# Performance work log

Hardware: AMD Instinct MI355X
Metric: run time of the kernel (lower is better)

## Reference

```python
import jax, jax.numpy as jnp
import numpy as np

B, T, D, H, HD, L, V = 2048, 64, 128, 4, 32, 6, 256
DFF = 4 * D
PARAM_NAMES = ['tok_emb', 'pos_emb', 'Wq', 'Wk', 'Wv', 'Wo', 'bo', 'ln1_g', 'ln1_b',
               'W1', 'b1', 'W2', 'b2', 'ln2_g', 'ln2_b', 'lnf_g', 'lnf_b', 'Wh', 'bh']


def setup_inputs() -> dict:
    key = jax.random.key(0)
    ks = jax.random.split(key, 12)
    def n(k, shape, s=0.02):
        return jax.random.normal(k, shape, jnp.float32) * s
    return dict(
        idx=jax.random.randint(ks[0], (B, T), 0, V),
        tok_emb=n(ks[1], (V, D)),
        pos_emb=n(ks[2], (T, D)),
        Wq=n(ks[3], (L, H, D, HD)),
        Wk=n(ks[4], (L, H, D, HD)),
        Wv=n(ks[5], (L, H, D, HD)),
        Wo=n(ks[6], (L, D, D)), bo=jnp.zeros((L, D), jnp.float32),
        ln1_g=jnp.ones((L, D), jnp.float32), ln1_b=jnp.zeros((L, D), jnp.float32),
        W1=n(ks[7], (L, D, DFF)), b1=jnp.zeros((L, DFF), jnp.float32),
        W2=n(ks[8], (L, DFF, D)), b2=jnp.zeros((L, D), jnp.float32),
        ln2_g=jnp.ones((L, D), jnp.float32), ln2_b=jnp.zeros((L, D), jnp.float32),
        lnf_g=jnp.ones((D,), jnp.float32), lnf_b=jnp.zeros((D,), jnp.float32),
        Wh=n(ks[9], (D, V)), bh=jnp.zeros((V,), jnp.float32),
    )


def _ln(x, g, b):
    m = x.mean(-1, keepdims=True)
    v = x.var(-1, keepdims=True)  # biased, matches torch LayerNorm
    return (x - m) / jnp.sqrt(v + 1e-5) * g + b


def _forward(idx, p):
    x = p['tok_emb'][idx] + p['pos_emb'][None, :, :]  # [B,T,D]
    mask = jnp.tril(jnp.ones((T, T), bool))

    def block(x, lp):
        Wq, Wk, Wv, Wo, bo, g1, bb1, W1, b1, W2, b2, g2, bb2 = lp
        h = _ln(x, g1, bb1)
        q = jnp.einsum('btd,hde->bhte', h, Wq)
        k = jnp.einsum('btd,hde->bhte', h, Wk)
        v = jnp.einsum('btd,hde->bhte', h, Wv)
        s = jnp.einsum('bhte,bhse->bhts', q, k) * (HD ** -0.5)
        s = jnp.where(mask, s, -jnp.inf)
        w = jax.nn.softmax(s, axis=-1)  # dropout inactive (eval mode)
        o = jnp.einsum('bhts,bhse->bthe', w, v).reshape(B, T, D)  # concat heads
        x = x + o @ Wo + bo
        h2 = _ln(x, g2, bb2)
        x = x + jax.nn.relu(h2 @ W1 + b1) @ W2 + b2
        return x, None

    lp = (p['Wq'], p['Wk'], p['Wv'], p['Wo'], p['bo'], p['ln1_g'], p['ln1_b'],
          p['W1'], p['b1'], p['W2'], p['b2'], p['ln2_g'], p['ln2_b'])
    x, _ = jax.lax.scan(block, x, lp)
    x = _ln(x, p['lnf_g'], p['lnf_b'])
    return x @ p['Wh'] + p['bh']  # [B,T,V] logits


def reference(idx, tok_emb, pos_emb, Wq, Wk, Wv, Wo, bo, ln1_g, ln1_b,
              W1, b1, W2, b2, ln2_g, ln2_b, lnf_g, lnf_b, Wh, bh):
    p = dict(zip(PARAM_NAMES, (tok_emb, pos_emb, Wq, Wk, Wv, Wo, bo, ln1_g, ln1_b,
                               W1, b1, W2, b2, ln2_g, ln2_b, lnf_g, lnf_b, Wh, bh)))
    return _forward(idx, p)
```

## Files before the change

### kernel.cpp

```cpp
#include <hip/hip_runtime.h>

typedef unsigned short ushort_t;
typedef __attribute__((ext_vector_type(8))) short short8;
typedef __attribute__((ext_vector_type(4))) float float4_;

#define B_   2048
#define T_   64
#define D_   128
#define H_   4
#define HD_  32
#define L_   6
#define V_   256
#define DFF_ 512
#define BT_  (B_*T_)

static __device__ __forceinline__ float b2f(ushort_t u) {
    return __uint_as_float(((unsigned int)u) << 16);
}
static __device__ __forceinline__ ushort_t f2b(float f) {
    unsigned int x = __float_as_uint(f);
    return (ushort_t)((x + 0x7fffu + ((x >> 16) & 1u)) >> 16);
}
static __device__ __forceinline__ int bf16_mode(const ushort_t* flag_src) {
    return flag_src[0] == 0x3F80;
}

#define AS1C(p) ((const __attribute__((address_space(1))) void*)(p))
#define AS3(p)  ((__attribute__((address_space(3))) void*)(p))

#define NCVT 19
struct Cvt {
    const void* src[NCVT];
    long base[NCVT];
    long total;
};

__global__ __launch_bounds__(256) void convert_all(
    Cvt c, ushort_t* __restrict__ dst, const ushort_t* __restrict__ flag_src)
{
    long i = (long)blockIdx.x * 256 + threadIdx.x;
    if (i >= c.total) return;
    int s = 0;
    #pragma unroll 1
    while (s + 1 < NCVT && i >= c.base[s + 1]) s++;
    long j = i - c.base[s];
    if (bf16_mode(flag_src))
        dst[i] = ((const ushort_t*)c.src[s])[j];
    else
        dst[i] = f2b(((const float*)c.src[s])[j]);
}

__global__ __launch_bounds__(256) void repack_qkv(
    const ushort_t* __restrict__ Wq, const ushort_t* __restrict__ Wk,
    const ushort_t* __restrict__ Wv, ushort_t* __restrict__ outw)
{
    int i = blockIdx.x * 256 + threadIdx.x;
    int d = i & 127;
    int c = (i >> 7) % 384;
    int l = i / (384 * 128);
    int sel = c >> 7, hh = (c >> 5) & 3, e = c & 31;
    const ushort_t* W = (sel == 0) ? Wq : (sel == 1) ? Wk : Wv;
    outw[i] = W[((l * 4 + hh) * 128 + d) * 32 + e];
}

__global__ __launch_bounds__(256) void transpose_w(
    const ushort_t* __restrict__ in, ushort_t* __restrict__ out, int K, int N)
{
    long i = (long)blockIdx.x * 256 + threadIdx.x;
    int n = (int)(i % N);
    int k = (int)((i / N) % K);
    int l = (int)(i / ((long)N * K));
    out[((long)l * N + n) * K + k] = in[i];
}

__global__ __launch_bounds__(256) void embed_ln_kernel(
    const int* __restrict__ idx, const ushort_t* __restrict__ tok,
    const ushort_t* __restrict__ pos, const ushort_t* __restrict__ g,
    const ushort_t* __restrict__ bta, float* __restrict__ x,
    ushort_t* __restrict__ hout)
{
    int row  = blockIdx.x * 4 + (threadIdx.x >> 6);
    int lane = threadIdx.x & 63;
    int t = row & 63;
    int id = idx[row];
    float v0 = b2f(tok[id * 128 + lane])      + b2f(pos[t * 128 + lane]);
    float v1 = b2f(tok[id * 128 + lane + 64]) + b2f(pos[t * 128 + lane + 64]);
    long o = (long)row * 128 + lane;
    x[o] = v0; x[o + 64] = v1;
    float s  = v0 + v1;
    float sq = v0 * v0 + v1 * v1;
    #pragma unroll
    for (int off = 1; off < 64; off <<= 1) {
        s  += __shfl_xor(s,  off);
        sq += __shfl_xor(sq, off);
    }
    float mean = s * (1.0f / 128.0f);
    float var  = sq * (1.0f / 128.0f) - mean * mean;
    float rstd = rsqrtf(var + 1e-5f);
    hout[o]      = f2b((v0 - mean) * rstd * b2f(g[lane])      + b2f(bta[lane]));
    hout[o + 64] = f2b((v1 - mean) * rstd * b2f(g[lane + 64]) + b2f(bta[lane + 64]));
}

__global__ __launch_bounds__(256) void gemm_bt(
    const ushort_t* __restrict__ A, const ushort_t* __restrict__ Bt,
    const ushort_t* __restrict__ bias, void* __restrict__ outp,
    const ushort_t* __restrict__ flag, int M, int N, int K, int relu)
{
    __shared__ __align__(16) ushort_t As[128 * 64];
    __shared__ __align__(16) ushort_t Bs[128 * 64];
    const int tid  = threadIdx.x;
    const int wave = tid >> 6, lane = tid & 63;
    const int wm = wave >> 1, wn = wave & 1;
    const int row0 = blockIdx.x * 128, col0 = blockIdx.y * 128;

    float4_ acc[4][4];
    #pragma unroll
    for (int m = 0; m < 4; m++)
        #pragma unroll
        for (int n = 0; n < 4; n++) acc[m][n] = (float4_)0.0f;

    const int srow = lane >> 3;
    const int scg  = (lane & 7) ^ srow;
    const int fr = lane & 15, fq = lane >> 4;

    for (int k0 = 0; k0 < K; k0 += 64) {
        __syncthreads();
        #pragma unroll
        for (int i = 0; i < 4; i++) {
            int chunk = wave * 4 + i;
            int r = chunk * 8 + srow;
            __builtin_amdgcn_global_load_lds(
                AS1C(&A[(size_t)(row0 + r) * K + k0 + scg * 8]),
                AS3(&As[chunk * 512]), 16, 0, 0);
            __builtin_amdgcn_global_load_lds(
                AS1C(&Bt[(size_t)(col0 + r) * K + k0 + scg * 8]),
                AS3(&Bs[chunk * 512]), 16, 0, 0);
        }
        __syncthreads();

        #pragma unroll
        for (int ks = 0; ks < 2; ks++) {
            short8 af[4], bf[4];
            #pragma unroll
            for (int mt = 0; mt < 4; mt++) {
                int r = wm * 64 + mt * 16 + fr;
                af[mt] = *(const short8*)&As[r * 64 + (((ks * 4 + fq) ^ (r & 7)) * 8)];
            }
            #pragma unroll
            for (int nt = 0; nt < 4; nt++) {
                int r = wn * 64 + nt * 16 + fr;
                bf[nt] = *(const short8*)&Bs[r * 64 + (((ks * 4 + fq) ^ (r & 7)) * 8)];
            }
            #pragma unroll
            for (int mt = 0; mt < 4; mt++)
                #pragma unroll
                for (int nt = 0; nt < 4; nt++)
                    acc[mt][nt] = __builtin_amdgcn_mfma_f32_16x16x32_bf16(
                        af[mt], bf[nt], acc[mt][nt], 0, 0, 0);
        }
    }

    const int out_bf16 = (flag == nullptr) || bf16_mode(flag);
    #pragma unroll
    for (int nt = 0; nt < 4; nt++) {
        int gcol = col0 + wn * 64 + nt * 16 + fr;
        float bb = bias ? b2f(bias[gcol]) : 0.0f;
        #pragma unroll
        for (int mt = 0; mt < 4; mt++) {
            #pragma unroll
            for (int i = 0; i < 4; i++) {
                int grow = row0 + wm * 64 + mt * 16 + fq * 4 + i;
                float v = acc[mt][nt][i] + bb;
                if (relu) v = fmaxf(v, 0.0f);
                long off = (long)grow * N + gcol;
                if (out_bf16) ((ushort_t*)outp)[off] = f2b(v);
                else          ((float*)outp)[off] = v;
            }
        }
    }
}

__global__ __launch_bounds__(256) void gemm_ln(
    const ushort_t* __restrict__ A, const ushort_t* __restrict__ Bt,
    const ushort_t* __restrict__ bias, float* __restrict__ x,
    const ushort_t* __restrict__ g, const ushort_t* __restrict__ bta,
    ushort_t* __restrict__ hout, int M, int K)
{
    __shared__ __align__(16) ushort_t As[128 * 64];
    __shared__ __align__(16) ushort_t Bs[128 * 64];
    __shared__ float stats[128][2][2];
    const int tid  = threadIdx.x;
    const int wave = tid >> 6, lane = tid & 63;
    const int wm = wave >> 1, wn = wave & 1;
    const int row0 = blockIdx.x * 128;
    const int N = 128;

    float4_ acc[4][4];
    #pragma unroll
    for (int m = 0; m < 4; m++)
        #pragma unroll
        for (int n = 0; n < 4; n++) acc[m][n] = (float4_)0.0f;

    const int srow = lane >> 3;
    const int scg  = (lane & 7) ^ srow;
    const int fr = lane & 15, fq = lane >> 4;

    for (int k0 = 0; k0 < K; k0 += 64) {
        __syncthreads();
        #pragma unroll
        for (int i = 0; i < 4; i++) {
            int chunk = wave * 4 + i;
            int r = chunk * 8 + srow;
            __builtin_amdgcn_global_load_lds(
                AS1C(&A[(size_t)(row0 + r) * K + k0 + scg * 8]),
                AS3(&As[chunk * 512]), 16, 0, 0);
            __builtin_amdgcn_global_load_lds(
                AS1C(&Bt[(size_t)r * K + k0 + scg * 8]),
                AS3(&Bs[chunk * 512]), 16, 0, 0);
        }
        __syncthreads();

        #pragma unroll
        for (int ks = 0; ks < 2; ks++) {
            short8 af[4], bf[4];
            #pragma unroll
            for (int mt = 0; mt < 4; mt++) {
                int r = wm * 64 + mt * 16 + fr;
                af[mt] = *(const short8*)&As[r * 64 + (((ks * 4 + fq) ^ (r & 7)) * 8)];
            }
            #pragma unroll
            for (int nt = 0; nt < 4; nt++) {
                int r = wn * 64 + nt * 16 + fr;
                bf[nt] = *(const short8*)&Bs[r * 64 + (((ks * 4 + fq) ^ (r & 7)) * 8)];
            }
            #pragma unroll
            for (int mt = 0; mt < 4; mt++)
                #pragma unroll
                for (int nt = 0; nt < 4; nt++)
                    acc[mt][nt] = __builtin_amdgcn_mfma_f32_16x16x32_bf16(
                        af[mt], bf[nt], acc[mt][nt], 0, 0, 0);
        }
    }

    int   col[4];
    float bbias[4], gg[4], bln[4];
    #pragma unroll
    for (int nt = 0; nt < 4; nt++) {
        col[nt]  = wn * 64 + nt * 16 + fr;
        bbias[nt] = b2f(bias[col[nt]]);
        gg[nt]    = b2f(g[col[nt]]);
        bln[nt]   = b2f(bta[col[nt]]);
    }
    #pragma unroll
    for (int mt = 0; mt < 4; mt++) {
        #pragma unroll
        for (int i = 0; i < 4; i++) {
            int lr = wm * 64 + mt * 16 + fq * 4 + i;
            long rbase = (long)(row0 + lr) * N;
            float s = 0.0f, sq = 0.0f;
            #pragma unroll
            for (int nt = 0; nt < 4; nt++) {
                float nx = x[rbase + col[nt]] + acc[mt][nt][i] + bbias[nt];
                x[rbase + col[nt]] = nx;
                acc[mt][nt][i] = nx;
                s += nx; sq += nx * nx;
            }
            s  += __shfl_xor(s, 1);  sq += __shfl_xor(sq, 1);
            s  += __shfl_xor(s, 2);  sq += __shfl_xor(sq, 2);
            s  += __shfl_xor(s, 4);  sq += __shfl_xor(sq, 4);
            s  += __shfl_xor(s, 8);  sq += __shfl_xor(sq, 8);
            if (fr == 0) { stats[lr][wn][0] = s; stats[lr][wn][1] = sq; }
        }
    }
    __syncthreads();
    #pragma unroll
    for (int mt = 0; mt < 4; mt++) {
        #pragma unroll
        for (int i = 0; i < 4; i++) {
            int lr = wm * 64 + mt * 16 + fq * 4 + i;
            float s  = stats[lr][0][0] + stats[lr][1][0];
            float sq = stats[lr][0][1] + stats[lr][1][1];
            float mean = s * (1.0f / 128.0f);
            float var  = sq * (1.0f / 128.0f) - mean * mean;
            float rstd = rsqrtf(var + 1e-5f);
            long rbase = (long)(row0 + lr) * N;
            #pragma unroll
            for (int nt = 0; nt < 4; nt++) {
                float nx = acc[mt][nt][i];
                hout[rbase + col[nt]] = f2b((nx - mean) * rstd * gg[nt] + bln[nt]);
            }
        }
    }
}

__global__ __launch_bounds__(256) void ffn_fused(
    const ushort_t* __restrict__ hin,
    const ushort_t* __restrict__ w1,
    const ushort_t* __restrict__ b1v,
    const ushort_t* __restrict__ w2,
    const ushort_t* __restrict__ b2v,
    float* __restrict__ x,
    const ushort_t* __restrict__ g, const ushort_t* __restrict__ bta,
    ushort_t* __restrict__ hout)
{
    __shared__ __align__(16) ushort_t Hs[128 * 128];
    __shared__ __align__(16) ushort_t Ms[128 * 128];
    __shared__ __align__(16) ushort_t Bs[128 * 64];
    const int tid  = threadIdx.x;
    const int wave = tid >> 6, lane = tid & 63;
    const int wm = wave >> 1, wn = wave & 1;
    const int row0 = blockIdx.x * 128;

    const int srow = lane >> 3;
    const int scg  = (lane & 7) ^ srow;
    const int fr = lane & 15, fq = lane >> 4;

    {
        int lr4 = lane >> 4, pg = lane & 15;
        #pragma unroll
        for (int i = 0; i < 8; i++) {
            int c = wave * 8 + i;
            int r = c * 4 + lr4;
            int kg = pg ^ (r & 7);
            __builtin_amdgcn_global_load_lds(
                AS1C(&hin[(size_t)(row0 + r) * 128 + kg * 8]),
                AS3(&Hs[c * 512]), 16, 0, 0);
        }
    }

    float4_ acc2[4][4];
    #pragma unroll
    for (int m = 0; m < 4; m++)
        #pragma unroll
        for (int n = 0; n < 4; n++) acc2[m][n] = (float4_)0.0f;

    #pragma unroll 1
    for (int c = 0; c < 4; c++) {
        const ushort_t* Wc = w1 + (size_t)c * 128 * 128;
        float4_ acc1[4][4];
        #pragma unroll
        for (int m = 0; m < 4; m++)
            #pragma unroll
            for (int n = 0; n < 4; n++) acc1[m][n] = (float4_)0.0f;

        #pragma unroll 1
        for (int k0 = 0; k0 < 128; k0 += 64) {
            __syncthreads();
            #pragma unroll
            for (int i = 0; i < 4; i++) {
                int chunk = wave * 4 + i;
                int r = chunk * 8 + srow;
                __builtin_amdgcn_global_load_lds(
                    AS1C(&Wc[(size_t)r * 128 + k0 + scg * 8]),
                    AS3(&Bs[chunk * 512]), 16, 0, 0);
            }
            __syncthreads();
            #pragma unroll
            for (int ks = 0; ks < 2; ks++) {
                int kb = (k0 >> 5) + ks;
                short8 af[4], bf[4];
                #pragma unroll
                for (int mt = 0; mt < 4; mt++) {
                    int r = wm * 64 + mt * 16 + fr;
                    af[mt] = *(const short8*)&Hs[r * 128 + (((kb * 4 + fq) ^ (r & 7)) * 8)];
                }
                #pragma unroll
                for (int nt = 0; nt < 4; nt++) {
                    int r = wn * 64 + nt * 16 + fr;
                    bf[nt] = *(const short8*)&Bs[r * 64 + (((ks * 4 + fq) ^ (r & 7)) * 8)];
                }
                #pragma unroll
                for (int mt = 0; mt < 4; mt++)
                    #pragma unroll
                    for (int nt = 0; nt < 4; nt++)
                        acc1[mt][nt] = __builtin_amdgcn_mfma_f32_16x16x32_bf16(
                            af[mt], bf[nt], acc1[mt][nt], 0, 0, 0);
            }
        }

        #pragma unroll
        for (int nt = 0; nt < 4; nt++) {
            int col = wn * 64 + nt * 16 + fr;
            float bb = b2f(b1v[c * 128 + col]);
            #pragma unroll
            for (int mt = 0; mt < 4; mt++) {
                #pragma unroll
                for (int i = 0; i < 4; i++) {
                    int row = wm * 64 + mt * 16 + fq * 4 + i;
                    float v = fmaxf(acc1[mt][nt][i] + bb, 0.0f);
                    Ms[row * 128 + (((col >> 3) ^ (row & 7)) * 8) + (col & 7)] = f2b(v);
                }
            }
        }

        #pragma unroll 1
        for (int k0 = 0; k0 < 128; k0 += 64) {
            __syncthreads();
            #pragma unroll
            for (int i = 0; i < 4; i++) {
                int chunk = wave * 4 + i;
                int r = chunk * 8 + srow;
                __builtin_amdgcn_global_load_lds(
                    AS1C(&w2[(size_t)r * 512 + c * 128 + k0 + scg * 8]),
                    AS3(&Bs[chunk * 512]), 16, 0, 0);
            }
            __syncthreads();
            #pragma unroll
            for (int ks = 0; ks < 2; ks++) {
                int kb = (k0 >> 5) + ks;
                short8 af[4], bf[4];
                #pragma unroll
                for (int mt = 0; mt < 4; mt++) {
                    int r = wm * 64 + mt * 16 + fr;
                    af[mt] = *(const short8*)&Ms[r * 128 + (((kb * 4 + fq) ^ (r & 7)) * 8)];
                }
                #pragma unroll
                for (int nt = 0; nt < 4; nt++) {
                    int r = wn * 64 + nt * 16 + fr;
                    bf[nt] = *(const short8*)&Bs[r * 64 + (((ks * 4 + fq) ^ (r & 7)) * 8)];
                }
                #pragma unroll
                for (int mt = 0; mt < 4; mt++)
                    #pragma unroll
                    for (int nt = 0; nt < 4; nt++)
                        acc2[mt][nt] = __builtin_amdgcn_mfma_f32_16x16x32_bf16(
                            af[mt], bf[nt], acc2[mt][nt], 0, 0, 0);
            }
        }
    }

    __syncthreads();
    float (*stats)[2][2] = (float (*)[2][2])(void*)Bs;
    int   col[4];
    float bbias[4], gg[4], bln[4];
    #pragma unroll
    for (int nt = 0; nt < 4; nt++) {
        col[nt]  = wn * 64 + nt * 16 + fr;
        bbias[nt] = b2f(b2v[col[nt]]);
        gg[nt]    = b2f(g[col[nt]]);
        bln[nt]   = b2f(bta[col[nt]]);
    }
    #pragma unroll
    for (int mt = 0; mt < 4; mt++) {
        #pragma unroll
        for (int i = 0; i < 4; i++) {
            int lr = wm * 64 + mt * 16 + fq * 4 + i;
            long rbase = (long)(row0 + lr) * 128;
            float s = 0.0f, sq = 0.0f;
            #pragma unroll
            for (int nt = 0; nt < 4; nt++) {
                float nx = x[rbase + col[nt]] + acc2[mt][nt][i] + bbias[nt];
                x[rbase + col[nt]] = nx;
                acc2[mt][nt][i] = nx;
                s += nx; sq += nx * nx;
            }
            s  += __shfl_xor(s, 1);  sq += __shfl_xor(sq, 1);
            s  += __shfl_xor(s, 2);  sq += __shfl_xor(sq, 2);
            s  += __shfl_xor(s, 4);  sq += __shfl_xor(sq, 4);
            s  += __shfl_xor(s, 8);  sq += __shfl_xor(sq, 8);
            if (fr == 0) { stats[lr][wn][0] = s; stats[lr][wn][1] = sq; }
        }
    }
    __syncthreads();
    #pragma unroll
    for (int mt = 0; mt < 4; mt++) {
        #pragma unroll
        for (int i = 0; i < 4; i++) {
            int lr = wm * 64 + mt * 16 + fq * 4 + i;
            float s  = stats[lr][0][0] + stats[lr][1][0];
            float sq = stats[lr][0][1] + stats[lr][1][1];
            float mean = s * (1.0f / 128.0f);
            float var  = sq * (1.0f / 128.0f) - mean * mean;
            float rstd = rsqrtf(var + 1e-5f);
            long rbase = (long)(row0 + lr) * 128;
            #pragma unroll
            for (int nt = 0; nt < 4; nt++) {
                float nx = acc2[mt][nt][i];
                hout[rbase + col[nt]] = f2b((nx - mean) * rstd * gg[nt] + bln[nt]);
            }
        }
    }
}

__global__ __launch_bounds__(256) void attn_kernel(
    const ushort_t* __restrict__ qkv,
    ushort_t* __restrict__ out)
{
    __shared__ __align__(16) ushort_t Qs[64][40];
    __shared__ __align__(16) ushort_t Ks[64][40];
    __shared__ __align__(16) ushort_t Vt[32][72];
    __shared__ __align__(16) ushort_t Pb[64][72];
    const int tid = threadIdx.x;
    const int b = blockIdx.x >> 2, h = blockIdx.x & 3;
    const long base = (long)b * T_ * 384 + h * 32;

    {
        int t = tid >> 2, e8 = (tid & 3) * 8;
        const ushort_t* p = &qkv[base + (long)t * 384 + e8];
        short8 qv = *(const short8*)(p);
        short8 kv = *(const short8*)(p + 128);
        short8 vv = *(const short8*)(p + 256);
        *(short8*)&Qs[t][e8] = qv;
        *(short8*)&Ks[t][e8] = kv;
        #pragma unroll
        for (int j = 0; j < 8; j++) Vt[e8 + j][t] = (ushort_t)vv[j];
    }
    __syncthreads();

    const int w = tid >> 6, lane = tid & 63, fr = lane & 15, fq = lane >> 4;

    short8 qf = *(const short8*)&Qs[w * 16 + fr][fq * 8];
    float4_ s[4];
    #pragma unroll
    for (int tj = 0; tj < 4; tj++) s[tj] = (float4_)0.0f;
    #pragma unroll
    for (int tj = 0; tj < 4; tj++) {
        if (tj <= w) {
            short8 kf = *(const short8*)&Ks[tj * 16 + fr][fq * 8];
            s[tj] = __builtin_amdgcn_mfma_f32_16x16x32_bf16(qf, kf, s[tj], 0, 0, 0);
        }
    }

    const float scale = 0.17677669529663687f;
    float pv[4][4];
    #pragma unroll
    for (int i = 0; i < 4; i++) {
        float mx = -1.0e30f;
        float vv4[4];
        int   ok[4];
        #pragma unroll
        for (int tj = 0; tj < 4; tj++) {
            ok[tj] = (tj < w) || (tj == w && fr <= fq * 4 + i);
            float v = ok[tj] ? s[tj][i] * scale : -1.0e30f;
            vv4[tj] = v;
            mx = fmaxf(mx, v);
        }
        mx = fmaxf(mx, __shfl_xor(mx, 1));
        mx = fmaxf(mx, __shfl_xor(mx, 2));
        mx = fmaxf(mx, __shfl_xor(mx, 4));
        mx = fmaxf(mx, __shfl_xor(mx, 8));
        float sm = 0.0f;
        #pragma unroll
        for (int tj = 0; tj < 4; tj++) {
            float e = ok[tj] ? __expf(vv4[tj] - mx) : 0.0f;
            vv4[tj] = e;
            sm += e;
        }
        sm += __shfl_xor(sm, 1);
        sm += __shfl_xor(sm, 2);
        sm += __shfl_xor(sm, 4);
        sm += __shfl_xor(sm, 8);
        float inv = 1.0f / sm;
        #pragma unroll
        for (int tj = 0; tj < 4; tj++) pv[i][tj] = vv4[tj] * inv;
    }
    #pragma unroll
    for (int tj = 0; tj < 4; tj++)
        #pragma unroll
        for (int i = 0; i < 4; i++)
            Pb[w * 16 + fq * 4 + i][tj * 16 + fr] = f2b(pv[i][tj]);
    __syncthreads();

    float4_ o[2];
    o[0] = (float4_)0.0f; o[1] = (float4_)0.0f;
    #pragma unroll
    for (int ks = 0; ks < 2; ks++) {
        short8 pf = *(const short8*)&Pb[w * 16 + fr][ks * 32 + fq * 8];
        #pragma unroll
        for (int nt = 0; nt < 2; nt++) {
            short8 vf = *(const short8*)&Vt[nt * 16 + fr][ks * 32 + fq * 8];
            o[nt] = __builtin_amdgcn_mfma_f32_16x16x32_bf16(pf, vf, o[nt], 0, 0, 0);
        }
    }
    #pragma unroll
    for (int nt = 0; nt < 2; nt++)
        #pragma unroll
        for (int i = 0; i < 4; i++)
            out[(long)(b * T_ + w * 16 + fq * 4 + i) * 128 + h * 32 + nt * 16 + fr]
                = f2b(o[nt][i]);
}

extern "C" void kernel_launch(void* const* d_in, const int* in_sizes, int n_in,
                              void* d_out, int out_size, void* d_ws, size_t ws_size,
                              hipStream_t stream)
{
    (void)in_sizes; (void)n_in; (void)out_size; (void)ws_size;
    const int* idx = (const int*)d_in[0];
    const ushort_t* flag = (const ushort_t*)d_in[8];

    char* ws = (char*)d_ws;
    float*    x    = (float*)ws;     ws += (size_t)BT_ * D_ * 4;
    ushort_t* h    = (ushort_t*)ws;  ws += (size_t)BT_ * D_ * 2;
    ushort_t* qkvb = (ushort_t*)ws;  ws += (size_t)BT_ * 384 * 2;
    ushort_t* ao   = (ushort_t*)ws;  ws += (size_t)BT_ * D_ * 2;
    ushort_t* wqkv = (ushort_t*)ws;  ws += (size_t)L_ * 384 * 128 * 2;
    ushort_t* wo   = (ushort_t*)ws;  ws += (size_t)L_ * 128 * 128 * 2;
    ushort_t* w1   = (ushort_t*)ws;  ws += (size_t)L_ * 512 * 128 * 2;
    ushort_t* w2   = (ushort_t*)ws;  ws += (size_t)L_ * 128 * 512 * 2;
    ushort_t* wh   = (ushort_t*)ws;  ws += (size_t)256 * 128 * 2;
    ushort_t* cvt  = (ushort_t*)ws;

    static const long cnt[NCVT] = {
        (long)V_*D_, (long)T_*D_,
        (long)L_*H_*D_*HD_, (long)L_*H_*D_*HD_, (long)L_*H_*D_*HD_,
        (long)L_*D_*D_, (long)L_*D_,
        (long)L_*D_, (long)L_*D_,
        (long)L_*D_*DFF_, (long)L_*DFF_,
        (long)L_*DFF_*D_, (long)L_*D_,
        (long)L_*D_, (long)L_*D_,
        (long)D_, (long)D_,
        (long)D_*V_, (long)V_
    };
    Cvt c;
    long off = 0;
    for (int i = 0; i < NCVT; i++) { c.src[i] = d_in[i + 1]; c.base[i] = off; off += cnt[i]; }
    c.total = off;
    ushort_t* ctok  = cvt + c.base[0];
    ushort_t* cpos  = cvt + c.base[1];
    ushort_t* cWq   = cvt + c.base[2];
    ushort_t* cWk   = cvt + c.base[3];
    ushort_t* cWv   = cvt + c.base[4];
    ushort_t* cWo   = cvt + c.base[5];
    ushort_t* cbo   = cvt + c.base[6];
    ushort_t* cln1g = cvt + c.base[7];
    ushort_t* cln1b = cvt + c.base[8];
    ushort_t* cW1   = cvt + c.base[9];
    ushort_t* cb1   = cvt + c.base[10];
    ushort_t* cW2   = cvt + c.base[11];
    ushort_t* cb2   = cvt + c.base[12];
    ushort_t* cln2g = cvt + c.base[13];
    ushort_t* cln2b = cvt + c.base[14];
    ushort_t* clnfg = cvt + c.base[15];
    ushort_t* clnfb = cvt + c.base[16];
    ushort_t* cWh   = cvt + c.base[17];
    ushort_t* cbh   = cvt + c.base[18];

    convert_all<<<(int)((c.total + 255) / 256), 256, 0, stream>>>(c, cvt, flag);

    repack_qkv <<<1152, 256, 0, stream>>>(cWq, cWk, cWv, wqkv);
    transpose_w<<<384,  256, 0, stream>>>(cWo, wo, 128, 128);
    transpose_w<<<1536, 256, 0, stream>>>(cW1, w1, 128, 512);
    transpose_w<<<1536, 256, 0, stream>>>(cW2, w2, 512, 128);
    transpose_w<<<128,  256, 0, stream>>>(cWh, wh, 128, 256);
    embed_ln_kernel<<<BT_ / 4, 256, 0, stream>>>(idx, ctok, cpos, cln1g, cln1b, x, h);

    for (int l = 0; l < L_; l++) {
        gemm_bt<<<dim3(BT_ / 128, 3), 256, 0, stream>>>(
            h, wqkv + l * 384 * 128, nullptr, qkvb, nullptr, BT_, 384, 128, 0);
        attn_kernel<<<B_ * H_, 256, 0, stream>>>(qkvb, ao);
        gemm_ln<<<BT_ / 128, 256, 0, stream>>>(
            ao, wo + l * 128 * 128, cbo + l * 128, x,
            cln2g + l * 128, cln2b + l * 128, h, BT_, 128);
        const ushort_t* ng = (l < L_ - 1) ? (cln1g + (l + 1) * 128) : clnfg;
        const ushort_t* nb = (l < L_ - 1) ? (cln1b + (l + 1) * 128) : clnfb;
        ffn_fused<<<BT_ / 128, 256, 0, stream>>>(
            h, w1 + l * 512 * 128, cb1 + l * 512,
            w2 + l * 128 * 512, cb2 + l * 128, x, ng, nb, h);
    }
    gemm_bt<<<dim3(BT_ / 128, 2), 256, 0, stream>>>(
        h, wh, cbh, d_out, flag, BT_, 256, 128, 0);
}
```

Baseline: 1.675 ms.

## Load weight fragments directly from global, stage full-K activations once in LDS

The GEMM kernels (gemm_bt, gemm_ln, and both GEMMs in ffn_fused) no longer stage weight tiles through LDS. Each wave now reads its B fragments straight from global memory, where the small weight matrices should stay cache-resident. In gemm_bt and gemm_ln the full 128-wide K slice of A is loaded into LDS once, replacing the per-64 K loop, which removes several barriers and LDS round trips per tile. The risk is higher global/L2 latency on the fragment loads with no prefetch, and the K=128 assumption is now hardcoded.

```diff
diff --git a/kernel.cpp b/kernel.cpp
--- a/kernel.cpp
+++ b/kernel.cpp
@@ -104,14 +104,28 @@
 __global__ __launch_bounds__(256) void gemm_bt(
     const ushort_t* __restrict__ A, const ushort_t* __restrict__ Bt,
     const ushort_t* __restrict__ bias, void* __restrict__ outp,
-    const ushort_t* __restrict__ flag, int M, int N, int K, int relu)
-{
-    __shared__ __align__(16) ushort_t As[128 * 64];
-    __shared__ __align__(16) ushort_t Bs[128 * 64];
+    const ushort_t* __restrict__ flag, int M, int N, int relu)
+{
+    __shared__ __align__(16) ushort_t As[128 * 128];
     const int tid  = threadIdx.x;
     const int wave = tid >> 6, lane = tid & 63;
     const int wm = wave >> 1, wn = wave & 1;
     const int row0 = blockIdx.x * 128, col0 = blockIdx.y * 128;
+    const int fr = lane & 15, fq = lane >> 4;
+    (void)M;
+
+    {
+        int lr4 = lane >> 4, pg = lane & 15;
+        #pragma unroll
+        for (int i = 0; i < 8; i++) {
+            int c = wave * 8 + i;
+            int r = c * 4 + lr4;
+            int kg = pg ^ (r & 7);
+            __builtin_amdgcn_global_load_lds(
+                AS1C(&A[(size_t)(row0 + r) * 128 + kg * 8]),
+                AS3(&As[c * 512]), 16, 0, 0);
+        }
+    }
 
     float4_ acc[4][4];
     #pragma unroll
@@ -119,45 +133,27 @@
         #pragma unroll
         for (int n = 0; n < 4; n++) acc[m][n] = (float4_)0.0f;
 
-    const int srow = lane >> 3;
-    const int scg  = (lane & 7) ^ srow;
-    const int fr = lane & 15, fq = lane >> 4;
-
-    for (int k0 = 0; k0 < K; k0 += 64) {
-        __syncthreads();
-        #pragma unroll
-        for (int i = 0; i < 4; i++) {
-            int chunk = wave * 4 + i;
-            int r = chunk * 8 + srow;
-            __builtin_amdgcn_global_load_lds(
-                AS1C(&A[(size_t)(row0 + r) * K + k0 + scg * 8]),
-                AS3(&As[chunk * 512]), 16, 0, 0);
-            __builtin_amdgcn_global_load_lds(
-                AS1C(&Bt[(size_t)(col0 + r) * K + k0 + scg * 8]),
-                AS3(&Bs[chunk * 512]), 16, 0, 0);
-        }
-        __syncthreads();
-
-        #pragma unroll
-        for (int ks = 0; ks < 2; ks++) {
-            short8 af[4], bf[4];
-            #pragma unroll
-            for (int mt = 0; mt < 4; mt++) {
-                int r = wm * 64 + mt * 16 + fr;
-                af[mt] = *(const short8*)&As[r * 64 + (((ks * 4 + fq) ^ (r & 7)) * 8)];
-            }
-            #pragma unroll
-            for (int nt = 0; nt < 4; nt++) {
-                int r = wn * 64 + nt * 16 + fr;
-                bf[nt] = *(const short8*)&Bs[r * 64 + (((ks * 4 + fq) ^ (r & 7)) * 8)];
-            }
-            #pragma unroll
-            for (int mt = 0; mt < 4; mt++)
-                #pragma unroll
-                for (int nt = 0; nt < 4; nt++)
-                    acc[mt][nt] = __builtin_amdgcn_mfma_f32_16x16x32_bf16(
-                        af[mt], bf[nt], acc[mt][nt], 0, 0, 0);
-        }
+    __syncthreads();
+
+    #pragma unroll
+    for (int kb = 0; kb < 4; kb++) {
+        short8 af[4], bf[4];
+        #pragma unroll
+        for (int nt = 0; nt < 4; nt++) {
+            int col = col0 + wn * 64 + nt * 16 + fr;
+            bf[nt] = *(const short8*)&Bt[(size_t)col * 128 + kb * 32 + fq * 8];
+        }
+        #pragma unroll
+        for (int mt = 0; mt < 4; mt++) {
+            int r = wm * 64 + mt * 16 + fr;
+            af[mt] = *(const short8*)&As[r * 128 + (((kb * 4 + fq) ^ (r & 7)) * 8)];
+        }
+        #pragma unroll
+        for (int mt = 0; mt < 4; mt++)
+            #pragma unroll
+            for (int nt = 0; nt < 4; nt++)
+                acc[mt][nt] = __builtin_amdgcn_mfma_f32_16x16x32_bf16(
+                    af[mt], bf[nt], acc[mt][nt], 0, 0, 0);
     }
 
     const int out_bf16 = (flag == nullptr) || bf16_mode(flag);
@@ -184,16 +180,30 @@
     const ushort_t* __restrict__ A, const ushort_t* __restrict__ Bt,
     const ushort_t* __restrict__ bias, float* __restrict__ x,
     const ushort_t* __restrict__ g, const ushort_t* __restrict__ bta,
-    ushort_t* __restrict__ hout, int M, int K)
-{
-    __shared__ __align__(16) ushort_t As[128 * 64];
-    __shared__ __align__(16) ushort_t Bs[128 * 64];
+    ushort_t* __restrict__ hout, int M)
+{
+    __shared__ __align__(16) ushort_t As[128 * 128];
     __shared__ float stats[128][2][2];
     const int tid  = threadIdx.x;
     const int wave = tid >> 6, lane = tid & 63;
     const int wm = wave >> 1, wn = wave & 1;
     const int row0 = blockIdx.x * 128;
     const int N = 128;
+    const int fr = lane & 15, fq = lane >> 4;
+    (void)M;
+
+    {
+        int lr4 = lane >> 4, pg = lane & 15;
+        #pragma unroll
+        for (int i = 0; i < 8; i++) {
+            int c = wave * 8 + i;
+            int r = c * 4 + lr4;
+            int kg = pg ^ (r & 7);
+            __builtin_amdgcn_global_load_lds(
+                AS1C(&A[(size_t)(row0 + r) * 128 + kg * 8]),
+                AS3(&As[c * 512]), 16, 0, 0);
+        }
+    }
 
     float4_ acc[4][4];
     #pragma unroll
@@ -201,45 +211,27 @@
         #pragma unroll
         for (int n = 0; n < 4; n++) acc[m][n] = (float4_)0.0f;
 
-    const int srow = lane >> 3;
-    const int scg  = (lane & 7) ^ srow;
-    const int fr = lane & 15, fq = lane >> 4;
-
-    for (int k0 = 0; k0 < K; k0 += 64) {
-        __syncthreads();
-        #pragma unroll
-        for (int i = 0; i < 4; i++) {
-            int chunk = wave * 4 + i;
-            int r = chunk * 8 + srow;
-            __builtin_amdgcn_global_load_lds(
-                AS1C(&A[(size_t)(row0 + r) * K + k0 + scg * 8]),
-                AS3(&As[chunk * 512]), 16, 0, 0);
-            __builtin_amdgcn_global_load_lds(
-                AS1C(&Bt[(size_t)r * K + k0 + scg * 8]),
-                AS3(&Bs[chunk * 512]), 16, 0, 0);
-        }
-        __syncthreads();
-
-        #pragma unroll
-        for (int ks = 0; ks < 2; ks++) {
-            short8 af[4], bf[4];
-            #pragma unroll
-            for (int mt = 0; mt < 4; mt++) {
-                int r = wm * 64 + mt * 16 + fr;
-                af[mt] = *(const short8*)&As[r * 64 + (((ks * 4 + fq) ^ (r & 7)) * 8)];
-            }
-            #pragma unroll
-            for (int nt = 0; nt < 4; nt++) {
-                int r = wn * 64 + nt * 16 + fr;
-                bf[nt] = *(const short8*)&Bs[r * 64 + (((ks * 4 + fq) ^ (r & 7)) * 8)];
-            }
-            #pragma unroll
-            for (int mt = 0; mt < 4; mt++)
-                #pragma unroll
-                for (int nt = 0; nt < 4; nt++)
-                    acc[mt][nt] = __builtin_amdgcn_mfma_f32_16x16x32_bf16(
-                        af[mt], bf[nt], acc[mt][nt], 0, 0, 0);
-        }
+    __syncthreads();
+
+    #pragma unroll
+    for (int kb = 0; kb < 4; kb++) {
+        short8 af[4], bf[4];
+        #pragma unroll
+        for (int nt = 0; nt < 4; nt++) {
+            int col = wn * 64 + nt * 16 + fr;
+            bf[nt] = *(const short8*)&Bt[(size_t)col * 128 + kb * 32 + fq * 8];
+        }
+        #pragma unroll
+        for (int mt = 0; mt < 4; mt++) {
+            int r = wm * 64 + mt * 16 + fr;
+            af[mt] = *(const short8*)&As[r * 128 + (((kb * 4 + fq) ^ (r & 7)) * 8)];
+        }
+        #pragma unroll
+        for (int mt = 0; mt < 4; mt++)
+            #pragma unroll
+            for (int nt = 0; nt < 4; nt++)
+                acc[mt][nt] = __builtin_amdgcn_mfma_f32_16x16x32_bf16(
+                    af[mt], bf[nt], acc[mt][nt], 0, 0, 0);
     }
 
     int   col[4];
@@ -305,14 +297,11 @@
 {
     __shared__ __align__(16) ushort_t Hs[128 * 128];
     __shared__ __align__(16) ushort_t Ms[128 * 128];
-    __shared__ __align__(16) ushort_t Bs[128 * 64];
+    __shared__ float stats[128][2][2];
     const int tid  = threadIdx.x;
     const int wave = tid >> 6, lane = tid & 63;
     const int wm = wave >> 1, wn = wave & 1;
     const int row0 = blockIdx.x * 128;
-
-    const int srow = lane >> 3;
-    const int scg  = (lane & 7) ^ srow;
     const int fr = lane & 15, fq = lane >> 4;
 
     {
@@ -334,6 +323,8 @@
         #pragma unroll
         for (int n = 0; n < 4; n++) acc2[m][n] = (float4_)0.0f;
 
+    __syncthreads();
+
     #pragma unroll 1
     for (int c = 0; c < 4; c++) {
         const ushort_t* Wc = w1 + (size_t)c * 128 * 128;
@@ -343,41 +334,28 @@
             #pragma unroll
             for (int n = 0; n < 4; n++) acc1[m][n] = (float4_)0.0f;
 
-        #pragma unroll 1
-        for (int k0 = 0; k0 < 128; k0 += 64) {
-            __syncthreads();
-            #pragma unroll
-            for (int i = 0; i < 4; i++) {
-                int chunk = wave * 4 + i;
-                int r = chunk * 8 + srow;
-                __builtin_amdgcn_global_load_lds(
-                    AS1C(&Wc[(size_t)r * 128 + k0 + scg * 8]),
-                    AS3(&Bs[chunk * 512]), 16, 0, 0);
-            }
-            __syncthreads();
-            #pragma unroll
-            for (int ks = 0; ks < 2; ks++) {
-                int kb = (k0 >> 5) + ks;
-                short8 af[4], bf[4];
+        #pragma unroll
+        for (int kb = 0; kb < 4; kb++) {
+            short8 af[4], bf[4];
+            #pragma unroll
+            for (int nt = 0; nt < 4; nt++) {
+                int col = wn * 64 + nt * 16 + fr;
+                bf[nt] = *(const short8*)&Wc[(size_t)col * 128 + kb * 32 + fq * 8];
+            }
+            #pragma unroll
+            for (int mt = 0; mt < 4; mt++) {
+                int r = wm * 64 + mt * 16 + fr;
+                af[mt] = *(const short8*)&Hs[r * 128 + (((kb * 4 + fq) ^ (r & 7)) * 8)];
+            }
+            #pragma unroll
+            for (int mt = 0; mt < 4; mt++)
                 #pragma unroll
-                for (int mt = 0; mt < 4; mt++) {
-                    int r = wm * 64 + mt * 16 + fr;
-                    af[mt] = *(const short8*)&Hs[r * 128 + (((kb * 4 + fq) ^ (r & 7)) * 8)];
-                }
-                #pragma unroll
-                for (int nt = 0; nt < 4; nt++) {
-                    int r = wn * 64 + nt * 16 + fr;
-                    bf[nt] = *(const short8*)&Bs[r * 64 + (((ks * 4 + fq) ^ (r & 7)) * 8)];
-                }
-                #pragma unroll
-                for (int mt = 0; mt < 4; mt++)
-                    #pragma unroll
-                    for (int nt = 0; nt < 4; nt++)
-                        acc1[mt][nt] = __builtin_amdgcn_mfma_f32_16x16x32_bf16(
-                            af[mt], bf[nt], acc1[mt][nt], 0, 0, 0);
-            }
-        }
-
+                for (int nt = 0; nt < 4; nt++)
+                    acc1[mt][nt] = __builtin_amdgcn_mfma_f32_16x16x32_bf16(
+                        af[mt], bf[nt], acc1[mt][nt], 0, 0, 0);
+        }
+
+        __syncthreads();
         #pragma unroll
         for (int nt = 0; nt < 4; nt++) {
             int col = wn * 64 + nt * 16 + fr;
@@ -392,45 +370,30 @@
                 }
             }
         }
-
-        #pragma unroll 1
-        for (int k0 = 0; k0 < 128; k0 += 64) {
-            __syncthreads();
-            #pragma unroll
-            for (int i = 0; i < 4; i++) {
-                int chunk = wave * 4 + i;
-                int r = chunk * 8 + srow;
-                __builtin_amdgcn_global_load_lds(
-                    AS1C(&w2[(size_t)r * 512 + c * 128 + k0 + scg * 8]),
-                    AS3(&Bs[chunk * 512]), 16, 0, 0);
-            }
-            __syncthreads();
-            #pragma unroll
-            for (int ks = 0; ks < 2; ks++) {
-                int kb = (k0 >> 5) + ks;
-                short8 af[4], bf[4];
+        __syncthreads();
+
+        #pragma unroll
+        for (int kb = 0; kb < 4; kb++) {
+            short8 af[4], bf[4];
+            #pragma unroll
+            for (int nt = 0; nt < 4; nt++) {
+                int col = wn * 64 + nt * 16 + fr;
+                bf[nt] = *(const short8*)&w2[(size_t)col * 512 + c * 128 + kb * 32 + fq * 8];
+            }
+            #pragma unroll
+            for (int mt = 0; mt < 4; mt++) {
+                int r = wm * 64 + mt * 16 + fr;
+                af[mt] = *(const short8*)&Ms[r * 128 + (((kb * 4 + fq) ^ (r & 7)) * 8)];
+            }
+            #pragma unroll
+            for (int mt = 0; mt < 4; mt++)
                 #pragma unroll
-                for (int mt = 0; mt < 4; mt++) {
-                    int r = wm * 64 + mt * 16 + fr;
-                    af[mt] = *(const short8*)&Ms[r * 128 + (((kb * 4 + fq) ^ (r & 7)) * 8)];
-                }
-                #pragma unroll
-                for (int nt = 0; nt < 4; nt++) {
-                    int r = wn * 64 + nt * 16 + fr;
-                    bf[nt] = *(const short8*)&Bs[r * 64 + (((ks * 4 + fq) ^ (r & 7)) * 8)];
-                }
-                #pragma unroll
-                for (int mt = 0; mt < 4; mt++)
-                    #pragma unroll
-                    for (int nt = 0; nt < 4; nt++)
-                        acc2[mt][nt] = __builtin_amdgcn_mfma_f32_16x16x32_bf16(
-                            af[mt], bf[nt], acc2[mt][nt], 0, 0, 0);
-            }
-        }
-    }
-
-    __syncthreads();
-    float (*stats)[2][2] = (float (*)[2][2])(void*)Bs;
+                for (int nt = 0; nt < 4; nt++)
+                    acc2[mt][nt] = __builtin_amdgcn_mfma_f32_16x16x32_bf16(
+                        af[mt], bf[nt], acc2[mt][nt], 0, 0, 0);
+        }
+    }
+
     int   col[4];
     float bbias[4], gg[4], bln[4];
     #pragma unroll
@@ -646,11 +609,11 @@
 
     for (int l = 0; l < L_; l++) {
         gemm_bt<<<dim3(BT_ / 128, 3), 256, 0, stream>>>(
-            h, wqkv + l * 384 * 128, nullptr, qkvb, nullptr, BT_, 384, 128, 0);
+            h, wqkv + l * 384 * 128, nullptr, qkvb, nullptr, BT_, 384, 0);
         attn_kernel<<<B_ * H_, 256, 0, stream>>>(qkvb, ao);
         gemm_ln<<<BT_ / 128, 256, 0, stream>>>(
             ao, wo + l * 128 * 128, cbo + l * 128, x,
-            cln2g + l * 128, cln2b + l * 128, h, BT_, 128);
+            cln2g + l * 128, cln2b + l * 128, h, BT_);
         const ushort_t* ng = (l < L_ - 1) ? (cln1g + (l + 1) * 128) : clnfg;
         const ushort_t* nb = (l < L_ - 1) ? (cln1b + (l + 1) * 128) : clnfb;
         ffn_fused<<<BT_ / 128, 256, 0, stream>>>(
@@ -658,5 +621,5 @@
             w2 + l * 128 * 512, cb2 + l * 128, x, ng, nb, h);
     }
     gemm_bt<<<dim3(BT_ / 128, 2), 256, 0, stream>>>(
-        h, wh, cbh, d_out, flag, BT_, 256, 128, 0);
-}
+        h, wh, cbh, d_out, flag, BT_, 256, 0);
+}
```

After: 1.807 ms. 7.9% more time.

## Fuse QKV projection, attention, output projection and LayerNorm into one kernel

Applied to the files above, without the earlier changes.

Replaces the per-layer QKV GEMM, attention kernel and Wo+residual+LayerNorm GEMM with a single kernel where each block handles one sequence (64 tokens). The block loops over the four heads, computing Q/K/V, causal softmax, P·V and accumulating the output projection in registers, then applies bias, residual and LayerNorm. This removes the qkv and attention-output intermediates from global memory and cuts two launches per layer. In exchange, weight fragments are read straight from global memory (no LDS staging), each head iteration adds barriers, and only 2048 blocks are launched. A __syncthreads is also added in ffn_fused.

```diff
diff --git a/kernel.cpp b/kernel.cpp
--- a/kernel.cpp
+++ b/kernel.cpp
@@ -180,116 +180,195 @@
     }
 }
 
-__global__ __launch_bounds__(256) void gemm_ln(
-    const ushort_t* __restrict__ A, const ushort_t* __restrict__ Bt,
-    const ushort_t* __restrict__ bias, float* __restrict__ x,
+__global__ __launch_bounds__(256) void attn_fused(
+    const ushort_t* __restrict__ hin,
+    const ushort_t* __restrict__ wqkv,
+    const ushort_t* __restrict__ wo,
+    const ushort_t* __restrict__ bo,
+    float* __restrict__ x,
     const ushort_t* __restrict__ g, const ushort_t* __restrict__ bta,
-    ushort_t* __restrict__ hout, int M, int K)
-{
-    __shared__ __align__(16) ushort_t As[128 * 64];
-    __shared__ __align__(16) ushort_t Bs[128 * 64];
-    __shared__ float stats[128][2][2];
-    const int tid  = threadIdx.x;
-    const int wave = tid >> 6, lane = tid & 63;
-    const int wm = wave >> 1, wn = wave & 1;
-    const int row0 = blockIdx.x * 128;
-    const int N = 128;
-
-    float4_ acc[4][4];
-    #pragma unroll
-    for (int m = 0; m < 4; m++)
-        #pragma unroll
-        for (int n = 0; n < 4; n++) acc[m][n] = (float4_)0.0f;
-
-    const int srow = lane >> 3;
-    const int scg  = (lane & 7) ^ srow;
+    ushort_t* __restrict__ hout)
+{
+    __shared__ __align__(16) ushort_t Hb[64 * 128];
+    __shared__ __align__(16) ushort_t QKP[5120];
+    __shared__ __align__(16) ushort_t Vt[32][72];
+    __shared__ __align__(16) ushort_t AoH[64][40];
+
+    ushort_t (*Qs)[40] = (ushort_t (*)[40])(void*)QKP;
+    ushort_t (*Ks)[40] = (ushort_t (*)[40])(void*)(QKP + 64 * 40);
+    ushort_t (*Pb)[72] = (ushort_t (*)[72])(void*)QKP;
+
+    const int tid = threadIdx.x;
+    const int w = tid >> 6, lane = tid & 63;
     const int fr = lane & 15, fq = lane >> 4;
-
-    for (int k0 = 0; k0 < K; k0 += 64) {
+    const long rowg0 = (long)blockIdx.x * 64;
+
+    {
+        int lr4 = lane >> 4, pg = lane & 15;
+        #pragma unroll
+        for (int i = 0; i < 4; i++) {
+            int c = w * 4 + i;
+            int r = c * 4 + lr4;
+            int kg = pg ^ (r & 7);
+            __builtin_amdgcn_global_load_lds(
+                AS1C(&hin[(rowg0 + r) * 128 + kg * 8]),
+                AS3(&Hb[c * 512]), 16, 0, 0);
+        }
+    }
+
+    float4_ accp[8];
+    #pragma unroll
+    for (int n = 0; n < 8; n++) accp[n] = (float4_)0.0f;
+
+    __syncthreads();
+
+    short8 af[4];
+    #pragma unroll
+    for (int kb = 0; kb < 4; kb++) {
+        int r = w * 16 + fr;
+        af[kb] = *(const short8*)&Hb[r * 128 + (((kb * 4 + fq) ^ (r & 7)) * 8)];
+    }
+
+    const float scale = 0.17677669529663687f;
+
+    #pragma unroll 1
+    for (int hh = 0; hh < 4; hh++) {
+        if (hh > 0) __syncthreads();
+
+        float4_ aq[2], ak[2], av[2];
+        #pragma unroll
+        for (int nt = 0; nt < 2; nt++) {
+            aq[nt] = (float4_)0.0f; ak[nt] = (float4_)0.0f; av[nt] = (float4_)0.0f;
+        }
+        #pragma unroll
+        for (int kb = 0; kb < 4; kb++) {
+            #pragma unroll
+            for (int nt = 0; nt < 2; nt++) {
+                int colq = hh * 32 + nt * 16 + fr;
+                short8 bq = *(const short8*)&wqkv[(size_t)colq * 128 + kb * 32 + fq * 8];
+                short8 bk = *(const short8*)&wqkv[(size_t)(colq + 128) * 128 + kb * 32 + fq * 8];
+                short8 bv = *(const short8*)&wqkv[(size_t)(colq + 256) * 128 + kb * 32 + fq * 8];
+                aq[nt] = __builtin_amdgcn_mfma_f32_16x16x32_bf16(af[kb], bq, aq[nt], 0, 0, 0);
+                ak[nt] = __builtin_amdgcn_mfma_f32_16x16x32_bf16(af[kb], bk, ak[nt], 0, 0, 0);
+                av[nt] = __builtin_amdgcn_mfma_f32_16x16x32_bf16(af[kb], bv, av[nt], 0, 0, 0);
+            }
+        }
+        #pragma unroll
+        for (int nt = 0; nt < 2; nt++)
+            #pragma unroll
+            for (int i = 0; i < 4; i++) {
+                int t = w * 16 + fq * 4 + i, e = nt * 16 + fr;
+                Qs[t][e] = f2b(aq[nt][i]);
+                Ks[t][e] = f2b(ak[nt][i]);
+                Vt[e][t] = f2b(av[nt][i]);
+            }
         __syncthreads();
+
+        short8 qf = *(const short8*)&Qs[w * 16 + fr][fq * 8];
+        float4_ s[4];
+        #pragma unroll
+        for (int tj = 0; tj < 4; tj++) s[tj] = (float4_)0.0f;
+        #pragma unroll
+        for (int tj = 0; tj < 4; tj++) {
+            if (tj <= w) {
+                short8 kf = *(const short8*)&Ks[tj * 16 + fr][fq * 8];
+                s[tj] = __builtin_amdgcn_mfma_f32_16x16x32_bf16(qf, kf, s[tj], 0, 0, 0);
+            }
+        }
+
+        float pv[4][4];
         #pragma unroll
         for (int i = 0; i < 4; i++) {
-            int chunk = wave * 4 + i;
-            int r = chunk * 8 + srow;
-            __builtin_amdgcn_global_load_lds(
-                AS1C(&A[(size_t)(row0 + r) * K + k0 + scg * 8]),
-                AS3(&As[chunk * 512]), 16, 0, 0);
-            __builtin_amdgcn_global_load_lds(
-                AS1C(&Bt[(size_t)r * K + k0 + scg * 8]),
-                AS3(&Bs[chunk * 512]), 16, 0, 0);
-        }
+            float mx = -1.0e30f;
+            float vv4[4];
+            int   ok[4];
+            #pragma unroll
+            for (int tj = 0; tj < 4; tj++) {
+                ok[tj] = (tj < w) || (tj == w && fr <= fq * 4 + i);
+                float v = ok[tj] ? s[tj][i] * scale : -1.0e30f;
+                vv4[tj] = v;
+                mx = fmaxf(mx, v);
+            }
+            mx = fmaxf(mx, __shfl_xor(mx, 1));
+            mx = fmaxf(mx, __shfl_xor(mx, 2));
+            mx = fmaxf(mx, __shfl_xor(mx, 4));
+            mx = fmaxf(mx, __shfl_xor(mx, 8));
+            float sm = 0.0f;
+            #pragma unroll
+            for (int tj = 0; tj < 4; tj++) {
+                float e = ok[tj] ? __expf(vv4[tj] - mx) : 0.0f;
+                vv4[tj] = e;
+                sm += e;
+            }
+            sm += __shfl_xor(sm, 1);
+            sm += __shfl_xor(sm, 2);
+            sm += __shfl_xor(sm, 4);
+            sm += __shfl_xor(sm, 8);
+            float inv = 1.0f / sm;
+            #pragma unroll
+            for (int tj = 0; tj < 4; tj++) pv[i][tj] = vv4[tj] * inv;
+        }
+
         __syncthreads();
 
         #pragma unroll
+        for (int tj = 0; tj < 4; tj++)
+            #pragma unroll
+            for (int i = 0; i < 4; i++)
+                Pb[w * 16 + fq * 4 + i][tj * 16 + fr] = f2b(pv[i][tj]);
+
+        float4_ o[2];
+        o[0] = (float4_)0.0f; o[1] = (float4_)0.0f;
+        #pragma unroll
         for (int ks = 0; ks < 2; ks++) {
-            short8 af[4], bf[4];
-            #pragma unroll
-            for (int mt = 0; mt < 4; mt++) {
-                int r = wm * 64 + mt * 16 + fr;
-                af[mt] = *(const short8*)&As[r * 64 + (((ks * 4 + fq) ^ (r & 7)) * 8)];
-            }
-            #pragma unroll
-            for (int nt = 0; nt < 4; nt++) {
-                int r = wn * 64 + nt * 16 + fr;
-                bf[nt] = *(const short8*)&Bs[r * 64 + (((ks * 4 + fq) ^ (r & 7)) * 8)];
-            }
-            #pragma unroll
-            for (int mt = 0; mt < 4; mt++)
-                #pragma unroll
-                for (int nt = 0; nt < 4; nt++)
-                    acc[mt][nt] = __builtin_amdgcn_mfma_f32_16x16x32_bf16(
-                        af[mt], bf[nt], acc[mt][nt], 0, 0, 0);
-        }
-    }
-
-    int   col[4];
-    float bbias[4], gg[4], bln[4];
-    #pragma unroll
-    for (int nt = 0; nt < 4; nt++) {
-        col[nt]  = wn * 64 + nt * 16 + fr;
-        bbias[nt] = b2f(bias[col[nt]]);
-        gg[nt]    = b2f(g[col[nt]]);
-        bln[nt]   = b2f(bta[col[nt]]);
-    }
-    #pragma unroll
-    for (int mt = 0; mt < 4; mt++) {
-        #pragma unroll
-        for (int i = 0; i < 4; i++) {
-            int lr = wm * 64 + mt * 16 + fq * 4 + i;
-            long rbase = (long)(row0 + lr) * N;
-            float s = 0.0f, sq = 0.0f;
-            #pragma unroll
-            for (int nt = 0; nt < 4; nt++) {
-                float nx = x[rbase + col[nt]] + acc[mt][nt][i] + bbias[nt];
-                x[rbase + col[nt]] = nx;
-                acc[mt][nt][i] = nx;
-                s += nx; sq += nx * nx;
-            }
-            s  += __shfl_xor(s, 1);  sq += __shfl_xor(sq, 1);
-            s  += __shfl_xor(s, 2);  sq += __shfl_xor(sq, 2);
-            s  += __shfl_xor(s, 4);  sq += __shfl_xor(sq, 4);
-            s  += __shfl_xor(s, 8);  sq += __shfl_xor(sq, 8);
-            if (fr == 0) { stats[lr][wn][0] = s; stats[lr][wn][1] = sq; }
-        }
-    }
-    __syncthreads();
-    #pragma unroll
-    for (int mt = 0; mt < 4; mt++) {
-        #pragma unroll
-        for (int i = 0; i < 4; i++) {
-            int lr = wm * 64 + mt * 16 + fq * 4 + i;
-            float s  = stats[lr][0][0] + stats[lr][1][0];
-            float sq = stats[lr][0][1] + stats[lr][1][1];
-            float mean = s * (1.0f / 128.0f);
-            float var  = sq * (1.0f / 128.0f) - mean * mean;
-            float rstd = rsqrtf(var + 1e-5f);
-            long rbase = (long)(row0 + lr) * N;
-            #pragma unroll
-            for (int nt = 0; nt < 4; nt++) {
-                float nx = acc[mt][nt][i];
-                hout[rbase + col[nt]] = f2b((nx - mean) * rstd * gg[nt] + bln[nt]);
-            }
-        }
+            short8 pf = *(const short8*)&Pb[w * 16 + fr][ks * 32 + fq * 8];
+            #pragma unroll
+            for (int nt = 0; nt < 2; nt++) {
+                short8 vf = *(const short8*)&Vt[nt * 16 + fr][ks * 32 + fq * 8];
+                o[nt] = __builtin_amdgcn_mfma_f32_16x16x32_bf16(pf, vf, o[nt], 0, 0, 0);
+            }
+        }
+        #pragma unroll
+        for (int nt = 0; nt < 2; nt++)
+            #pragma unroll
+            for (int i = 0; i < 4; i++)
+                AoH[w * 16 + fq * 4 + i][nt * 16 + fr] = f2b(o[nt][i]);
+
+        short8 afp = *(const short8*)&AoH[w * 16 + fr][fq * 8];
+        #pragma unroll
+        for (int n = 0; n < 8; n++) {
+            short8 bfp = *(const short8*)&wo[(size_t)(n * 16 + fr) * 128 + hh * 32 + fq * 8];
+            accp[n] = __builtin_amdgcn_mfma_f32_16x16x32_bf16(afp, bfp, accp[n], 0, 0, 0);
+        }
+    }
+
+    float bb[8], gg[8], bl[8];
+    #pragma unroll
+    for (int n = 0; n < 8; n++) {
+        int c = n * 16 + fr;
+        bb[n] = b2f(bo[c]); gg[n] = b2f(g[c]); bl[n] = b2f(bta[c]);
+    }
+    #pragma unroll
+    for (int i = 0; i < 4; i++) {
+        long rbase = (rowg0 + w * 16 + fq * 4 + i) * 128;
+        float nx[8];
+        float s = 0.0f, sq = 0.0f;
+        #pragma unroll
+        for (int n = 0; n < 8; n++) {
+            float v = x[rbase + n * 16 + fr] + accp[n][i] + bb[n];
+            x[rbase + n * 16 + fr] = v;
+            nx[n] = v; s += v; sq += v * v;
+        }
+        s += __shfl_xor(s, 1);  sq += __shfl_xor(sq, 1);
+        s += __shfl_xor(s, 2);  sq += __shfl_xor(sq, 2);
+        s += __shfl_xor(s, 4);  sq += __shfl_xor(sq, 4);
+        s += __shfl_xor(s, 8);  sq += __shfl_xor(sq, 8);
+        float mean = s * (1.0f / 128.0f);
+        float var  = sq * (1.0f / 128.0f) - mean * mean;
+        float rstd = rsqrtf(var + 1e-5f);
+        #pragma unroll
+        for (int n = 0; n < 8; n++)
+            hout[rbase + n * 16 + fr] = f2b((nx[n] - mean) * rstd * gg[n] + bl[n]);
     }
 }
 
@@ -378,6 +457,7 @@
             }
         }
 
+        __syncthreads();
         #pragma unroll
         for (int nt = 0; nt < 4; nt++) {
             int col = wn * 64 + nt * 16 + fr;
@@ -482,104 +562,6 @@
     }
 }
 
-__global__ __launch_bounds__(256) void attn_kernel(
-    const ushort_t* __restrict__ qkv,
-    ushort_t* __restrict__ out)
-{
-    __shared__ __align__(16) ushort_t Qs[64][40];
-    __shared__ __align__(16) ushort_t Ks[64][40];
-    __shared__ __align__(16) ushort_t Vt[32][72];
-    __shared__ __align__(16) ushort_t Pb[64][72];
-    const int tid = threadIdx.x;
-    const int b = blockIdx.x >> 2, h = blockIdx.x & 3;
-    const long base = (long)b * T_ * 384 + h * 32;
-
-    {
-        int t = tid >> 2, e8 = (tid & 3) * 8;
-        const ushort_t* p = &qkv[base + (long)t * 384 + e8];
-        short8 qv = *(const short8*)(p);
-        short8 kv = *(const short8*)(p + 128);
-        short8 vv = *(const short8*)(p + 256);
-        *(short8*)&Qs[t][e8] = qv;
-        *(short8*)&Ks[t][e8] = kv;
-        #pragma unroll
-        for (int j = 0; j < 8; j++) Vt[e8 + j][t] = (ushort_t)vv[j];
-    }
-    __syncthreads();
-
-    const int w = tid >> 6, lane = tid & 63, fr = lane & 15, fq = lane >> 4;
-
-    short8 qf = *(const short8*)&Qs[w * 16 + fr][fq * 8];
-    float4_ s[4];
-    #pragma unroll
-    for (int tj = 0; tj < 4; tj++) s[tj] = (float4_)0.0f;
-    #pragma unroll
-    for (int tj = 0; tj < 4; tj++) {
-        if (tj <= w) {
-            short8 kf = *(const short8*)&Ks[tj * 16 + fr][fq * 8];
-            s[tj] = __builtin_amdgcn_mfma_f32_16x16x32_bf16(qf, kf, s[tj], 0, 0, 0);
-        }
-    }
-
-    const float scale = 0.17677669529663687f;
-    float pv[4][4];
-    #pragma unroll
-    for (int i = 0; i < 4; i++) {
-        float mx = -1.0e30f;
-        float vv4[4];
-        int   ok[4];
-        #pragma unroll
-        for (int tj = 0; tj < 4; tj++) {
-            ok[tj] = (tj < w) || (tj == w && fr <= fq * 4 + i);
-            float v = ok[tj] ? s[tj][i] * scale : -1.0e30f;
-            vv4[tj] = v;
-            mx = fmaxf(mx, v);
-        }
-        mx = fmaxf(mx, __shfl_xor(mx, 1));
-        mx = fmaxf(mx, __shfl_xor(mx, 2));
-        mx = fmaxf(mx, __shfl_xor(mx, 4));
-        mx = fmaxf(mx, __shfl_xor(mx, 8));
-        float sm = 0.0f;
-        #pragma unroll
-        for (int tj = 0; tj < 4; tj++) {
-            float e = ok[tj] ? __expf(vv4[tj] - mx) : 0.0f;
-            vv4[tj] = e;
-            sm += e;
-        }
-        sm += __shfl_xor(sm, 1);
-        sm += __shfl_xor(sm, 2);
-        sm += __shfl_xor(sm, 4);
-        sm += __shfl_xor(sm, 8);
-        float inv = 1.0f / sm;
-        #pragma unroll
-        for (int tj = 0; tj < 4; tj++) pv[i][tj] = vv4[tj] * inv;
-    }
-    #pragma unroll
-    for (int tj = 0; tj < 4; tj++)
-        #pragma unroll
-        for (int i = 0; i < 4; i++)
-            Pb[w * 16 + fq * 4 + i][tj * 16 + fr] = f2b(pv[i][tj]);
-    __syncthreads();
-
-    float4_ o[2];
-    o[0] = (float4_)0.0f; o[1] = (float4_)0.0f;
-    #pragma unroll
-    for (int ks = 0; ks < 2; ks++) {
-        short8 pf = *(const short8*)&Pb[w * 16 + fr][ks * 32 + fq * 8];
-        #pragma unroll
-        for (int nt = 0; nt < 2; nt++) {
-            short8 vf = *(const short8*)&Vt[nt * 16 + fr][ks * 32 + fq * 8];
-            o[nt] = __builtin_amdgcn_mfma_f32_16x16x32_bf16(pf, vf, o[nt], 0, 0, 0);
-        }
-    }
-    #pragma unroll
-    for (int nt = 0; nt < 2; nt++)
-        #pragma unroll
-        for (int i = 0; i < 4; i++)
-            out[(long)(b * T_ + w * 16 + fq * 4 + i) * 128 + h * 32 + nt * 16 + fr]
-                = f2b(o[nt][i]);
-}
-
 extern "C" void kernel_launch(void* const* d_in, const int* in_sizes, int n_in,
                               void* d_out, int out_size, void* d_ws, size_t ws_size,
                               hipStream_t stream)
@@ -591,8 +573,6 @@
     char* ws = (char*)d_ws;
     float*    x    = (float*)ws;     ws += (size_t)BT_ * D_ * 4;
     ushort_t* h    = (ushort_t*)ws;  ws += (size_t)BT_ * D_ * 2;
-    ushort_t* qkvb = (ushort_t*)ws;  ws += (size_t)BT_ * 384 * 2;
-    ushort_t* ao   = (ushort_t*)ws;  ws += (size_t)BT_ * D_ * 2;
     ushort_t* wqkv = (ushort_t*)ws;  ws += (size_t)L_ * 384 * 128 * 2;
     ushort_t* wo   = (ushort_t*)ws;  ws += (size_t)L_ * 128 * 128 * 2;
     ushort_t* w1   = (ushort_t*)ws;  ws += (size_t)L_ * 512 * 128 * 2;
@@ -645,12 +625,9 @@
     embed_ln_kernel<<<BT_ / 4, 256, 0, stream>>>(idx, ctok, cpos, cln1g, cln1b, x, h);
 
     for (int l = 0; l < L_; l++) {
-        gemm_bt<<<dim3(BT_ / 128, 3), 256, 0, stream>>>(
-            h, wqkv + l * 384 * 128, nullptr, qkvb, nullptr, BT_, 384, 128, 0);
-        attn_kernel<<<B_ * H_, 256, 0, stream>>>(qkvb, ao);
-        gemm_ln<<<BT_ / 128, 256, 0, stream>>>(
-            ao, wo + l * 128 * 128, cbo + l * 128, x,
-            cln2g + l * 128, cln2b + l * 128, h, BT_, 128);
+        attn_fused<<<B_, 256, 0, stream>>>(
+            h, wqkv + l * 384 * 128, wo + l * 128 * 128, cbo + l * 128,
+            x, cln2g + l * 128, cln2b + l * 128, h);
         const ushort_t* ng = (l < L_ - 1) ? (cln1g + (l + 1) * 128) : clnfg;
         const ushort_t* nb = (l < L_ - 1) ? (cln1b + (l + 1) * 128) : clnfb;
         ffn_fused<<<BT_ / 128, 256, 0, stream>>>(
```

Measured after the change: 1.856 ms. 1.11x slower.
